# Kernel tuning notes

Measured on AMD Instinct MI355X. Metric: run time of the kernel, lower is better.

Reference implementation:

```python
import jax, jax.numpy as jnp
import numpy as np

N, FIN, H, F = 4096, 512, 4, 64  # nodes, in_dim, heads, out_dim per head


def setup_inputs() -> dict:
    key = jax.random.key(0)
    k1, k2, k3, k4, k5 = jax.random.split(key, 5)
    X = jax.random.normal(k1, (N, FIN), dtype=jnp.float32)
    A = jax.random.randint(k2, (N, N), 0, 2, dtype=jnp.int32)
    # params (torch uses xavier_uniform; scaled normals are fine for a numeric baseline)
    W = jax.random.normal(k3, (FIN, H * F), dtype=jnp.float32) * (1.0 / np.sqrt(FIN))
    a_src = jax.random.normal(k4, (H, F), dtype=jnp.float32) * (1.0 / np.sqrt(F))
    a_dst = jax.random.normal(k5, (H, F), dtype=jnp.float32) * (1.0 / np.sqrt(F))
    return {"X": X, "A": A, "W": W, "a_src": a_src, "a_dst": a_dst}


def reference(X, A, W, a_src, a_dst):
    negative_slope = 0.2
    A_mask = A != 0                                   # [N, N] bool
    XW = (X @ W).reshape(N, H, F)                     # [N, H, F]
    f1 = jnp.einsum("nhf,hf->hn", XW, a_src)          # [H, N] (src scores)
    f2 = jnp.einsum("nhf,hf->hn", XW, a_dst)          # [H, N] (dst scores)
    e = f1[:, :, None] + f2[:, None, :]               # [H, N, N]
    e = jnp.where(e > 0, e, negative_slope * e)       # leaky relu
    neg_inf = jnp.finfo(e.dtype).min
    e = jnp.where(A_mask[None, :, :], e, neg_inf)     # mask non-edges
    attn = jax.nn.softmax(e, axis=-1)                 # [H, N, N]
    h = jnp.einsum("hij,jhf->ihf", attn, XW)          # [N, H, F]
    h = h.reshape(N, H * F)
    return jax.nn.elu(h)
```

## Files before the change

kernel.cpp:

```cpp
#include <hip/hip_runtime.h>
#include <hip/hip_bf16.h>


#define NN   4096
#define FIN  512
#define H    4
#define F    64
#define HF   256
#define LOG2E 1.44269504088896340736f

typedef __attribute__((ext_vector_type(4))) float f32x4;
typedef __attribute__((ext_vector_type(8))) short short8;

union U8 { short8 s; unsigned int w[4]; };

__global__ __launch_bounds__(256) void gemm_scores_pack(
        const float* __restrict__ X, const float* __restrict__ W,
        const float* __restrict__ a_src, const float* __restrict__ a_dst,
        const int* __restrict__ A,
        float* __restrict__ f1h, float* __restrict__ f2h,
        unsigned short* __restrict__ Vhi,
        unsigned long long* __restrict__ Ab) {
    if (blockIdx.x >= 256) {
        const int pb   = blockIdx.x - 256;
        const int gw   = (pb * 256 + threadIdx.x) >> 6;
        const int lane = threadIdx.x & 63;
        const int nchunk = NN * NN / 64;
        for (int c = gw; c < nchunk; c += 4096) {
            int a = A[(size_t)c * 64 + lane];
            unsigned long long m = __ballot(a != 0);
            if (lane == 0) Ab[c] = m;
        }
        return;
    }

    __shared__ float Xs[32][64];
    __shared__ float Ws[32][64];
    __shared__ unsigned short Vt[64][72];

    const int bi = blockIdx.x & 63, h = blockIdx.x >> 6;
    const int t  = threadIdx.x;
    const int tx = t & 15, ty = t >> 4;

    float acc[4][4];
#pragma unroll
    for (int r = 0; r < 4; ++r)
#pragma unroll
        for (int c = 0; c < 4; ++c) acc[r][c] = 0.f;

    const int xr = t >> 2, xk = (t & 3) * 8;
    const int wk = t >> 3, wn = (t & 7) * 8;

    const float* Xp = X + (size_t)(bi * 64 + xr) * FIN + xk;
    const float* Wp = W + (size_t)wk * HF + h * F + wn;

    for (int k0 = 0; k0 < FIN; k0 += 32) {
        float4 xv0 = *(const float4*)(Xp + k0);
        float4 xv1 = *(const float4*)(Xp + k0 + 4);
        float4 wv0 = *(const float4*)(Wp + (size_t)k0 * HF);
        float4 wv1 = *(const float4*)(Wp + (size_t)k0 * HF + 4);
        __syncthreads();
        Xs[xk + 0][xr] = xv0.x; Xs[xk + 1][xr] = xv0.y;
        Xs[xk + 2][xr] = xv0.z; Xs[xk + 3][xr] = xv0.w;
        Xs[xk + 4][xr] = xv1.x; Xs[xk + 5][xr] = xv1.y;
        Xs[xk + 6][xr] = xv1.z; Xs[xk + 7][xr] = xv1.w;
        *(float4*)&Ws[wk][wn] = wv0;
        *(float4*)&Ws[wk][wn + 4] = wv1;
        __syncthreads();
#pragma unroll
        for (int kk = 0; kk < 32; ++kk) {
            float4 a4 = *(const float4*)&Xs[kk][ty * 4];
            float4 b4 = *(const float4*)&Ws[kk][tx * 4];
            float av[4] = {a4.x, a4.y, a4.z, a4.w};
            float bv[4] = {b4.x, b4.y, b4.z, b4.w};
#pragma unroll
            for (int r = 0; r < 4; ++r)
#pragma unroll
                for (int c = 0; c < 4; ++c) acc[r][c] += av[r] * bv[c];
        }
    }

    float4 as4 = *(const float4*)(a_src + h * F + tx * 4);
    float4 ad4 = *(const float4*)(a_dst + h * F + tx * 4);
    float asv[4] = {as4.x, as4.y, as4.z, as4.w};
    float adv[4] = {ad4.x, ad4.y, ad4.z, ad4.w};
#pragma unroll
    for (int r = 0; r < 4; ++r) {
        float s1 = 0.f, s2 = 0.f;
#pragma unroll
        for (int c = 0; c < 4; ++c) { s1 += acc[r][c] * asv[c]; s2 += acc[r][c] * adv[c]; }
#pragma unroll
        for (int off = 1; off < 16; off <<= 1) {
            s1 += __shfl_xor(s1, off, 16);
            s2 += __shfl_xor(s2, off, 16);
        }
        if (tx == 0) {
            const int n = bi * 64 + ty * 4 + r;
            f1h[h * NN + n] = s1 * LOG2E;
            f2h[h * NN + n] = s2 * LOG2E;
        }
    }

    __syncthreads();
#pragma unroll
    for (int r = 0; r < 4; ++r)
#pragma unroll
        for (int c = 0; c < 4; ++c) {
            __hip_bfloat16 b = __float2bfloat16(acc[r][c]);
            Vt[tx * 4 + c][ty * 4 + r] = __builtin_bit_cast(unsigned short, b);
        }
    __syncthreads();
    {
        const int f = t >> 2, ch = t & 3;
        short8 v0 = *(const short8*)&Vt[f][ch * 16];
        short8 v1 = *(const short8*)&Vt[f][ch * 16 + 8];
        unsigned short* dst = Vhi + (size_t)(h * F + f) * NN + bi * 64 + ch * 16;
        *(short8*)dst = v0;
        *(short8*)(dst + 8) = v1;
    }
}

template <int JLEN>
__global__ __launch_bounds__(256) void gat_attn_mfma(
        const unsigned int* __restrict__ Ab32,
        const unsigned short* __restrict__ Vhi,
        const float* __restrict__ f1h, const float* __restrict__ f2h,
        float* __restrict__ pacc, float* __restrict__ plsum) {
    constexpr int NCC = JLEN / 32;
    const int ib = blockIdx.x, jb = blockIdx.y;
    const int h    = threadIdx.x >> 6;
    const int lane = threadIdx.x & 63;
    const int il = lane & 15;
    const int kg = lane >> 4;
    const int sh = kg * 8;
    const int ibase = ib * 64 + il;

    float c[4];
#pragma unroll
    for (int rt = 0; rt < 4; ++rt) c[rt] = f1h[h * NN + ibase + rt * 16];

    const unsigned int* abp[4];
#pragma unroll
    for (int rt = 0; rt < 4; ++rt)
        abp[rt] = Ab32 + (size_t)(ibase + rt * 16) * (NN / 32) + jb * (JLEN / 32);

    const float* f2b = f2h + (size_t)h * NN + jb * JLEN + sh;

    const unsigned short* vb[4];
#pragma unroll
    for (int ft = 0; ft < 4; ++ft)
        vb[ft] = Vhi + (size_t)(h * F + ft * 16 + il) * NN + jb * JLEN + sh;

    f32x4 acc[4][4], lac[4];
#pragma unroll
    for (int rt = 0; rt < 4; ++rt) {
        lac[rt] = (f32x4){0.f, 0.f, 0.f, 0.f};
#pragma unroll
        for (int ft = 0; ft < 4; ++ft) acc[rt][ft] = (f32x4){0.f, 0.f, 0.f, 0.f};
    }

    short8 ones;
#pragma unroll
    for (int e = 0; e < 8; ++e) ones[e] = (short)0x3F80;

#pragma unroll 2
    for (int cc = 0; cc < NCC; ++cc) {
        unsigned int m[4];
#pragma unroll
        for (int rt = 0; rt < 4; ++rt) m[rt] = abp[rt][cc] >> sh;

        float4 ga = *(const float4*)(f2b + cc * 32);
        float4 gb = *(const float4*)(f2b + cc * 32 + 4);
        float gv[8] = {ga.x, ga.y, ga.z, ga.w, gb.x, gb.y, gb.z, gb.w};

        short8 bh[4];
#pragma unroll
        for (int ft = 0; ft < 4; ++ft)
            bh[ft] = *reinterpret_cast<const short8*>(vb[ft] + cc * 32);

#pragma unroll
        for (int rt = 0; rt < 4; ++rt) {
            float pf[8];
#pragma unroll
            for (int e = 0; e < 8; ++e) {
                float s = c[rt] + gv[e];
                s = fmaxf(s, 0.2f * s);
                float q = __builtin_amdgcn_exp2f(s);
                pf[e] = ((m[rt] >> e) & 1u) ? q : 0.f;
            }
            U8 pa;
#pragma unroll
            for (int e = 0; e < 8; e += 2)
                pa.w[e >> 1] = __builtin_amdgcn_perm(__float_as_uint(pf[e + 1]),
                                                     __float_as_uint(pf[e]),
                                                     0x07060302u);
#pragma unroll
            for (int ft = 0; ft < 4; ++ft)
                acc[rt][ft] = __builtin_amdgcn_mfma_f32_16x16x32_bf16(
                    pa.s, bh[ft], acc[rt][ft], 0, 0, 0);
            lac[rt] = __builtin_amdgcn_mfma_f32_16x16x32_bf16(
                pa.s, ones, lac[rt], 0, 0, 0);
        }
    }

    float* pb = pacc + (size_t)jb * NN * HF + (size_t)(ib * 64) * HF;
#pragma unroll
    for (int rt = 0; rt < 4; ++rt)
#pragma unroll
        for (int ft = 0; ft < 4; ++ft)
#pragma unroll
            for (int r = 0; r < 4; ++r)
                pb[(rt * 16 + kg * 4 + r) * HF + h * F + ft * 16 + il] = acc[rt][ft][r];

    if (il == 0) {
#pragma unroll
        for (int rt = 0; rt < 4; ++rt)
#pragma unroll
            for (int r = 0; r < 4; ++r)
                plsum[(size_t)jb * NN * H
                      + (size_t)(ib * 64 + rt * 16 + kg * 4 + r) * H + h] = lac[rt][r];
    }
}

__global__ __launch_bounds__(256) void finalize(
        const float* __restrict__ pacc, const float* __restrict__ plsum,
        const unsigned short* __restrict__ Vhi, float* __restrict__ out,
        int njb) {
    const int gid4 = blockIdx.x * 256 + threadIdx.x;
    const int i = gid4 >> 6, q = gid4 & 63;
    const int h = q >> 4;
    float4 a = make_float4(0.f, 0.f, 0.f, 0.f);
    float l = 0.f;
    for (int jb = 0; jb < njb; ++jb) {
        float4 p = *(const float4*)&pacc[(size_t)jb * NN * HF + (size_t)i * HF + q * 4];
        a.x += p.x; a.y += p.y; a.z += p.z; a.w += p.w;
        l += plsum[(size_t)jb * NN * H + (size_t)i * H + h];
    }
    float av[4] = {a.x, a.y, a.z, a.w};
    if (l == 0.f) {
#pragma unroll
        for (int c = 0; c < 4; ++c) {
            const unsigned short* col = Vhi + (size_t)(q * 4 + c) * NN;
            float s = 0.f;
            for (int j = 0; j < NN; ++j)
                s += __uint_as_float(((unsigned int)col[j]) << 16);
            av[c] = s;
        }
        l = (float)NN;
    }
    const float rl = 1.0f / l;
    float4 o;
    float* op = &o.x;
#pragma unroll
    for (int c = 0; c < 4; ++c) {
        float v = av[c] * rl;
        op[c] = (v > 0.f) ? v : (__builtin_amdgcn_exp2f(v * LOG2E) - 1.f);
    }
    *(float4*)&out[(size_t)i * HF + q * 4] = o;
}

extern "C" void kernel_launch(void* const* d_in, const int* in_sizes, int n_in,
                              void* d_out, int out_size, void* d_ws, size_t ws_size,
                              hipStream_t stream) {
    const float* X     = (const float*)d_in[0];
    const int*   A     = (const int*)d_in[1];
    const float* W     = (const float*)d_in[2];
    const float* a_src = (const float*)d_in[3];
    const float* a_dst = (const float*)d_in[4];
    float* out = (float*)d_out;

    const size_t fixed = (size_t)2 * NN * H * 4 + (size_t)HF * NN * 2
                       + (size_t)NN * NN / 8;
    auto need = [&](int njb) {
        return (size_t)njb * NN * HF * 4 + (size_t)njb * NN * H * 4 + fixed;
    };
    const int njb = (ws_size >= need(8)) ? 8 : 4;

    float* pacc = (float*)d_ws;
    float* f1h  = pacc + (size_t)njb * NN * HF;
    float* f2h  = f1h + (size_t)NN * H;
    unsigned short* Vhi = (unsigned short*)(f2h + (size_t)NN * H);
    float* plsum = (float*)(Vhi + (size_t)HF * NN);
    unsigned long long* Ab = (unsigned long long*)(plsum + (size_t)njb * NN * H);

    gemm_scores_pack<<<1280, 256, 0, stream>>>(X, W, a_src, a_dst, A,
                                               f1h, f2h, Vhi, Ab);
    if (njb == 8)
        gat_attn_mfma<512><<<dim3(64, 8), 256, 0, stream>>>(
            (const unsigned int*)Ab, Vhi, f1h, f2h, pacc, plsum);
    else
        gat_attn_mfma<1024><<<dim3(64, 4), 256, 0, stream>>>(
            (const unsigned int*)Ab, Vhi, f1h, f2h, pacc, plsum);
    finalize<<<NN * HF / 4 / 256, 256, 0, stream>>>(pacc, plsum, Vhi, out, njb);
}
```

Baseline: 71.17 us.

## Compute X@W projection with split-bf16 MFMA instead of FP32 SIMT tiling

Replaces the LDS-tiled FP32 FMA GEMM in the projection/score kernel with bf16 MFMA instructions, using a hi/lo split (three MFMAs per tile: hi*hi, hi*lo, lo*hi) to keep near-FP32 accuracy. A new pre-kernel transposes W and splits it into bf16 high and low halves in workspace. X is split on the fly in registers. Each block now handles 16 rows across all four heads with no shared memory. The cost is an extra kernel launch and workspace, plus uncoalesced scalar bf16 stores when writing the transposed V.

```diff
diff --git a/kernel.cpp b/kernel.cpp
--- a/kernel.cpp
+++ b/kernel.cpp
@@ -14,8 +14,29 @@
 
 union U8 { short8 s; unsigned int w[4]; };
 
+__global__ __launch_bounds__(256) void wt_split(
+        const float* __restrict__ W, unsigned short* __restrict__ Wth,
+        unsigned short* __restrict__ Wtl) {
+    const int gid = blockIdx.x * 256 + threadIdx.x;
+    const int hf = gid >> 6;
+    const int k0 = (gid & 63) * 8;
+    unsigned short h8[8], l8[8];
+#pragma unroll
+    for (int e = 0; e < 8; ++e) {
+        float x = W[(size_t)(k0 + e) * HF + hf];
+        unsigned u = __float_as_uint(x);
+        float lo = x - __uint_as_float(u & 0xFFFF0000u);
+        h8[e] = (unsigned short)(u >> 16);
+        l8[e] = (unsigned short)(__float_as_uint(lo) >> 16);
+    }
+    *(short8*)&Wth[(size_t)hf * FIN + k0] = *(const short8*)h8;
+    *(short8*)&Wtl[(size_t)hf * FIN + k0] = *(const short8*)l8;
+}
+
 __global__ __launch_bounds__(256) void gemm_scores_pack(
-        const float* __restrict__ X, const float* __restrict__ W,
+        const float* __restrict__ X,
+        const unsigned short* __restrict__ Wth,
+        const unsigned short* __restrict__ Wtl,
         const float* __restrict__ a_src, const float* __restrict__ a_dst,
         const int* __restrict__ A,
         float* __restrict__ f1h, float* __restrict__ f2h,
@@ -34,90 +55,70 @@
         return;
     }
 
-    __shared__ float Xs[32][64];
-    __shared__ float Ws[32][64];
-    __shared__ unsigned short Vt[64][72];
-
-    const int bi = blockIdx.x & 63, h = blockIdx.x >> 6;
-    const int t  = threadIdx.x;
-    const int tx = t & 15, ty = t >> 4;
-
-    float acc[4][4];
-#pragma unroll
-    for (int r = 0; r < 4; ++r)
-#pragma unroll
-        for (int c = 0; c < 4; ++c) acc[r][c] = 0.f;
-
-    const int xr = t >> 2, xk = (t & 3) * 8;
-    const int wk = t >> 3, wn = (t & 7) * 8;
-
-    const float* Xp = X + (size_t)(bi * 64 + xr) * FIN + xk;
-    const float* Wp = W + (size_t)wk * HF + h * F + wn;
-
+    const int h    = threadIdx.x >> 6;
+    const int lane = threadIdx.x & 63;
+    const int il = lane & 15;
+    const int kg = lane >> 4;
+    const int i0 = blockIdx.x * 16;
+
+    const float* xrow = X + (size_t)(i0 + il) * FIN + kg * 8;
+    const unsigned short* wh = Wth + (size_t)(h * F + il) * FIN + kg * 8;
+    const unsigned short* wl = Wtl + (size_t)(h * F + il) * FIN + kg * 8;
+
+    f32x4 acc[4];
+#pragma unroll
+    for (int ft = 0; ft < 4; ++ft) acc[ft] = (f32x4){0.f, 0.f, 0.f, 0.f};
+
+#pragma unroll 2
     for (int k0 = 0; k0 < FIN; k0 += 32) {
-        float4 xv0 = *(const float4*)(Xp + k0);
-        float4 xv1 = *(const float4*)(Xp + k0 + 4);
-        float4 wv0 = *(const float4*)(Wp + (size_t)k0 * HF);
-        float4 wv1 = *(const float4*)(Wp + (size_t)k0 * HF + 4);
-        __syncthreads();
-        Xs[xk + 0][xr] = xv0.x; Xs[xk + 1][xr] = xv0.y;
-        Xs[xk + 2][xr] = xv0.z; Xs[xk + 3][xr] = xv0.w;
-        Xs[xk + 4][xr] = xv1.x; Xs[xk + 5][xr] = xv1.y;
-        Xs[xk + 6][xr] = xv1.z; Xs[xk + 7][xr] = xv1.w;
-        *(float4*)&Ws[wk][wn] = wv0;
-        *(float4*)&Ws[wk][wn + 4] = wv1;
-        __syncthreads();
-#pragma unroll
-        for (int kk = 0; kk < 32; ++kk) {
-            float4 a4 = *(const float4*)&Xs[kk][ty * 4];
-            float4 b4 = *(const float4*)&Ws[kk][tx * 4];
-            float av[4] = {a4.x, a4.y, a4.z, a4.w};
-            float bv[4] = {b4.x, b4.y, b4.z, b4.w};
-#pragma unroll
-            for (int r = 0; r < 4; ++r)
-#pragma unroll
-                for (int c = 0; c < 4; ++c) acc[r][c] += av[r] * bv[c];
-        }
-    }
-
-    float4 as4 = *(const float4*)(a_src + h * F + tx * 4);
-    float4 ad4 = *(const float4*)(a_dst + h * F + tx * 4);
-    float asv[4] = {as4.x, as4.y, as4.z, as4.w};
-    float adv[4] = {ad4.x, ad4.y, ad4.z, ad4.w};
-#pragma unroll
-    for (int r = 0; r < 4; ++r) {
-        float s1 = 0.f, s2 = 0.f;
-#pragma unroll
-        for (int c = 0; c < 4; ++c) { s1 += acc[r][c] * asv[c]; s2 += acc[r][c] * adv[c]; }
-#pragma unroll
-        for (int off = 1; off < 16; off <<= 1) {
-            s1 += __shfl_xor(s1, off, 16);
-            s2 += __shfl_xor(s2, off, 16);
-        }
-        if (tx == 0) {
-            const int n = bi * 64 + ty * 4 + r;
-            f1h[h * NN + n] = s1 * LOG2E;
-            f2h[h * NN + n] = s2 * LOG2E;
-        }
-    }
-
-    __syncthreads();
-#pragma unroll
-    for (int r = 0; r < 4; ++r)
-#pragma unroll
-        for (int c = 0; c < 4; ++c) {
-            __hip_bfloat16 b = __float2bfloat16(acc[r][c]);
-            Vt[tx * 4 + c][ty * 4 + r] = __builtin_bit_cast(unsigned short, b);
-        }
-    __syncthreads();
-    {
-        const int f = t >> 2, ch = t & 3;
-        short8 v0 = *(const short8*)&Vt[f][ch * 16];
-        short8 v1 = *(const short8*)&Vt[f][ch * 16 + 8];
-        unsigned short* dst = Vhi + (size_t)(h * F + f) * NN + bi * 64 + ch * 16;
-        *(short8*)dst = v0;
-        *(short8*)(dst + 8) = v1;
-    }
+        float4 x0 = *(const float4*)(xrow + k0);
+        float4 x1 = *(const float4*)(xrow + k0 + 4);
+        float xs[8] = {x0.x, x0.y, x0.z, x0.w, x1.x, x1.y, x1.z, x1.w};
+        U8 xh, xl;
+#pragma unroll
+        for (int e = 0; e < 8; e += 2) {
+            unsigned ua = __float_as_uint(xs[e]), ub = __float_as_uint(xs[e + 1]);
+            xh.w[e >> 1] = __builtin_amdgcn_perm(ub, ua, 0x07060302u);
+            float la = xs[e]     - __uint_as_float(ua & 0xFFFF0000u);
+            float lb = xs[e + 1] - __uint_as_float(ub & 0xFFFF0000u);
+            xl.w[e >> 1] = __builtin_amdgcn_perm(__float_as_uint(lb),
+                                                 __float_as_uint(la), 0x07060302u);
+        }
+#pragma unroll
+        for (int ft = 0; ft < 4; ++ft) {
+            short8 ah = *(const short8*)(wh + (size_t)ft * 16 * FIN + k0);
+            short8 al = *(const short8*)(wl + (size_t)ft * 16 * FIN + k0);
+            acc[ft] = __builtin_amdgcn_mfma_f32_16x16x32_bf16(ah, xh.s, acc[ft], 0, 0, 0);
+            acc[ft] = __builtin_amdgcn_mfma_f32_16x16x32_bf16(ah, xl.s, acc[ft], 0, 0, 0);
+            acc[ft] = __builtin_amdgcn_mfma_f32_16x16x32_bf16(al, xh.s, acc[ft], 0, 0, 0);
+        }
+    }
+
+    float s1 = 0.f, s2 = 0.f;
+#pragma unroll
+    for (int ft = 0; ft < 4; ++ft) {
+        float4 a1 = *(const float4*)(a_src + h * F + ft * 16 + kg * 4);
+        float4 a2 = *(const float4*)(a_dst + h * F + ft * 16 + kg * 4);
+        s1 += acc[ft][0] * a1.x + acc[ft][1] * a1.y
+            + acc[ft][2] * a1.z + acc[ft][3] * a1.w;
+        s2 += acc[ft][0] * a2.x + acc[ft][1] * a2.y
+            + acc[ft][2] * a2.z + acc[ft][3] * a2.w;
+    }
+    s1 += __shfl_xor(s1, 16, 64); s1 += __shfl_xor(s1, 32, 64);
+    s2 += __shfl_xor(s2, 16, 64); s2 += __shfl_xor(s2, 32, 64);
+    if (kg == 0) {
+        f1h[h * NN + i0 + il] = s1 * LOG2E;
+        f2h[h * NN + i0 + il] = s2 * LOG2E;
+    }
+
+#pragma unroll
+    for (int ft = 0; ft < 4; ++ft)
+#pragma unroll
+        for (int r = 0; r < 4; ++r) {
+            __hip_bfloat16 b = __float2bfloat16(acc[ft][r]);
+            Vhi[(size_t)(h * F + ft * 16 + kg * 4 + r) * NN + i0 + il] =
+                __builtin_bit_cast(unsigned short, b);
+        }
 }
 
 template <int JLEN>
@@ -270,7 +271,7 @@
     float* out = (float*)d_out;
 
     const size_t fixed = (size_t)2 * NN * H * 4 + (size_t)HF * NN * 2
-                       + (size_t)NN * NN / 8;
+                       + (size_t)NN * NN / 8 + (size_t)2 * HF * FIN * 2;
     auto need = [&](int njb) {
         return (size_t)njb * NN * HF * 4 + (size_t)njb * NN * H * 4 + fixed;
     };
@@ -282,8 +283,11 @@
     unsigned short* Vhi = (unsigned short*)(f2h + (size_t)NN * H);
     float* plsum = (float*)(Vhi + (size_t)HF * NN);
     unsigned long long* Ab = (unsigned long long*)(plsum + (size_t)njb * NN * H);
-
-    gemm_scores_pack<<<1280, 256, 0, stream>>>(X, W, a_src, a_dst, A,
+    unsigned short* Wth = (unsigned short*)(Ab + (size_t)NN * NN / 64);
+    unsigned short* Wtl = Wth + (size_t)HF * FIN;
+
+    wt_split<<<64, 256, 0, stream>>>(W, Wth, Wtl);
+    gemm_scores_pack<<<1280, 256, 0, stream>>>(X, Wth, Wtl, a_src, a_dst, A,
                                                f1h, f2h, Vhi, Ab);
     if (njb == 8)
         gat_attn_mfma<512><<<dim3(64, 8), 256, 0, stream>>>(
```

Result: slower. 87.02 us (+22.3%).
